# Optimization experiments

Measured on AMD Instinct MI355X. Metric: run time of the kernel, lower is better.

Reference implementation:

```python
import jax, jax.numpy as jnp
import numpy as np

B, L, H, N = 4, 4096, 1024, 16
EPS = 1e-6  # layer_norm_epsilon


def setup_inputs() -> dict:
    key = jax.random.key(0)
    ks = jax.random.split(key, 8)
    hidden_states = jax.random.normal(ks[0], (B, L, H), dtype=jnp.float32)
    attention_mask = jnp.ones((B, L), dtype=jnp.float32)
    norm_weight = jnp.ones((H,), dtype=jnp.float32)
    # S4D init: dt log-uniform in [1e-3, 1e-1]; S4D-Lin A init; random C, D
    dt_min, dt_max = 1e-3, 1e-1
    log_dt = jax.random.uniform(ks[1], (H,), dtype=jnp.float32) * (
        float(np.log(dt_max)) - float(np.log(dt_min))) + float(np.log(dt_min))
    log_A_real = jnp.log(0.5 * jnp.ones((H, N), dtype=jnp.float32))
    A_imag = jnp.broadcast_to(float(np.pi) * jnp.arange(N, dtype=jnp.float32), (H, N))
    C_real = jax.random.normal(ks[2], (H, N), dtype=jnp.float32) * (0.5 ** 0.5)
    C_imag = jax.random.normal(ks[3], (H, N), dtype=jnp.float32) * (0.5 ** 0.5)
    D = jax.random.normal(ks[4], (H,), dtype=jnp.float32)
    out_w = jax.random.normal(ks[5], (2 * H, H), dtype=jnp.float32) * 0.02  # 1x1 conv to 2H (GLU)
    out_b = jnp.zeros((2 * H,), dtype=jnp.float32)
    return dict(hidden_states=hidden_states, attention_mask=attention_mask,
                norm_weight=norm_weight, log_dt=log_dt, log_A_real=log_A_real,
                A_imag=A_imag, C_real=C_real, C_imag=C_imag, D=D,
                out_w=out_w, out_b=out_b)


def _s4d_kernel(log_dt, log_A_real, A_imag, C_real, C_imag, length):
    """Diagonal SSM convolution kernel k[h, l] (S4D ZOH discretization)."""
    dt = jnp.exp(log_dt)                                   # (H,)
    A = -jnp.exp(log_A_real) + 1j * A_imag                 # (H, N) complex64
    C = C_real + 1j * C_imag                               # (H, N)
    dtA = A * dt[:, None]                                  # (H, N)
    C_disc = C * (jnp.exp(dtA) - 1.0) / A                  # (H, N)
    vand = jnp.exp(dtA[:, :, None] * jnp.arange(length, dtype=jnp.float32))  # (H, N, L)
    k = 2.0 * jnp.einsum('hn,hnl->hl', C_disc, vand).real  # (H, L)
    return k.astype(jnp.float32)


def reference(hidden_states, attention_mask, norm_weight, log_dt, log_A_real,
              A_imag, C_real, C_imag, D, out_w, out_b):
    # LongT5LayerNorm: RMSNorm (no mean subtraction), variance in fp32
    var = jnp.mean(jnp.square(hidden_states.astype(jnp.float32)), axis=-1, keepdims=True)
    normed = hidden_states * jax.lax.rsqrt(var + EPS) * norm_weight  # (B, L, H)
    # mask padded positions, go to channel-major layout (B, H, L)
    u = (normed * attention_mask[..., None]).transpose(0, 2, 1)
    Lx = u.shape[-1]
    k = _s4d_kernel(log_dt, log_A_real, A_imag, C_real, C_imag, Lx)  # (H, L)
    # causal convolution via FFT of length 2L
    nfft = 2 * Lx
    k_f = jnp.fft.rfft(k, n=nfft)                 # (H, nfft//2+1)
    u_f = jnp.fft.rfft(u, n=nfft)                 # (B, H, nfft//2+1)
    y = jnp.fft.irfft(u_f * k_f, n=nfft)[..., :Lx]  # (B, H, L)
    y = y + u * D[:, None]                        # skip connection
    y = jax.nn.gelu(y, approximate=False)         # torch nn.GELU (exact)
    # output 1x1 conv to 2H, then GLU over the channel dim
    z = jnp.einsum('bhl,oh->bol', y, out_w) + out_b[:, None]
    a, b = jnp.split(z, 2, axis=1)
    ssm_out = (a * jax.nn.sigmoid(b)).transpose(0, 2, 1)  # (B, L, H)
    # residual + dropout (eval mode -> identity)
    return hidden_states + ssm_out
```

## Files before the change

kernel.cpp:

```cpp
#include <hip/hip_runtime.h>

#define B_   4
#define L_   4096
#define H_   1024
#define N_   16
#define CH_  64
#define NC_  (L_/CH_)
#define M_   (B_*L_)
#define O2_  (2*H_)
#define EPS_ 1e-6f

typedef __attribute__((ext_vector_type(4))) float  f32x4;
typedef __attribute__((ext_vector_type(8))) __bf16 bf16x8;

__device__ __forceinline__ unsigned short f2bf(float x) {
  union { float f; unsigned int u; } v; v.f = x;
  unsigned int r = v.u + 0x7FFFu + ((v.u >> 16) & 1u);
  return (unsigned short)(r >> 16);
}
__device__ __forceinline__ float bf2f(unsigned short x) {
  union { unsigned int u; float f; } v; v.u = ((unsigned int)x) << 16;
  return v.f;
}

__device__ __forceinline__ void async_copy16(const void* g, void* l) {
  __builtin_amdgcn_global_load_lds(
      (const __attribute__((address_space(1))) unsigned int*)g,
      (__attribute__((address_space(3))) unsigned int*)l, 16, 0, 0);
}

__global__ void k_prep(const float* __restrict__ log_dt,
                       const float* __restrict__ log_A_real,
                       const float* __restrict__ A_imag,
                       const float* __restrict__ C_real,
                       const float* __restrict__ C_imag,
                       const float* __restrict__ outw,
                       const float* __restrict__ outb,
                       float* __restrict__ wr,  float* __restrict__ wi,
                       float* __restrict__ c2r, float* __restrict__ c2i,
                       float* __restrict__ wpr, float* __restrict__ wpi,
                       unsigned short* __restrict__ Wbf,
                       float* __restrict__ bp) {
  int idx = blockIdx.x * 256 + threadIdx.x;
  int p = idx >> 10, hh = idx & (H_ - 1);
  size_t src = (size_t)((p >> 1) + (p & 1) * H_) * H_ + hh;
  Wbf[idx] = f2bf(outw[src]);
  if (idx < O2_) bp[idx] = outb[(idx >> 1) + (idx & 1) * H_];
  if (idx < H_ * N_) {
    int h = idx / N_, n = idx % N_;
    int hn = h * N_ + n;
    float dt  = expf(log_dt[h]);
    float Ar  = -expf(log_A_real[hn]);
    float Ai  = A_imag[hn];
    float dr  = Ar * dt, di = Ai * dt;
    float er  = expf(dr);
    float wrv = er * cosf(di), wiv = er * sinf(di);
    float e1r = wrv - 1.0f, e1i = wiv;
    float den = Ar * Ar + Ai * Ai;
    float qr  = (e1r * Ar + e1i * Ai) / den;
    float qi  = (e1i * Ar - e1r * Ai) / den;
    float Cr  = C_real[hn], Ci = C_imag[hn];
    float cdr = Cr * qr - Ci * qi;
    float cdi = Cr * qi + Ci * qr;
    float ep  = expf((float)CH_ * dr);
    int o = n * H_ + h;
    wr[o]  = wrv;  wi[o]  = wiv;
    c2r[o] = 2.0f * cdr; c2i[o] = 2.0f * cdi;
    wpr[o] = ep * cosf((float)CH_ * di);
    wpi[o] = ep * sinf((float)CH_ * di);
  }
}

__global__ __launch_bounds__(256) void k_scale(const float* __restrict__ hs,
                                               const float* __restrict__ mask,
                                               float* __restrict__ scale) {
  int m = blockIdx.x, tid = threadIdx.x;
  float4 v = reinterpret_cast<const float4*>(hs + (size_t)m * H_)[tid];
  float s = v.x * v.x + v.y * v.y + v.z * v.z + v.w * v.w;
  #pragma unroll
  for (int off = 32; off > 0; off >>= 1) s += __shfl_down(s, off, 64);
  __shared__ float ps[4];
  if ((tid & 63) == 0) ps[tid >> 6] = s;
  __syncthreads();
  if (tid == 0) {
    float var = (ps[0] + ps[1] + ps[2] + ps[3]) * (1.0f / H_);
    scale[m] = rsqrtf(var + EPS_) * mask[m];
  }
}

__global__ __launch_bounds__(256) void k_scan1(const float* __restrict__ hs,
                                               const float* __restrict__ nw,
                                               const float* __restrict__ scale,
                                               const float* __restrict__ wr_,
                                               const float* __restrict__ wi_,
                                               float* __restrict__ endr,
                                               float* __restrict__ endi,
                                               unsigned short* __restrict__ ubf) {
  int tid = threadIdx.x;
  int h = blockIdx.x * 256 + tid;
  int c = blockIdx.y, b = blockIdx.z;
  float wr[N_], wi[N_], xr[N_], xi[N_];
  #pragma unroll
  for (int n = 0; n < N_; n++) {
    wr[n] = wr_[n * H_ + h]; wi[n] = wi_[n * H_ + h];
    xr[n] = 0.f; xi[n] = 0.f;
  }
  float nwh = nw[h];
  int l0 = c * CH_;
  const float* scp = scale + (size_t)b * L_ + l0;
  const float* hp = hs + ((size_t)b * L_ + l0) * H_ + h;
  unsigned short* up = ubf + ((size_t)b * L_ + l0) * H_ + h;
  #pragma unroll 8
  for (int l = 0; l < CH_; l++) {
    float u = hp[(size_t)l * H_] * scp[l] * nwh;
    unsigned short ub = f2bf(u);
    up[(size_t)l * H_] = ub;
    u = bf2f(ub);
    #pragma unroll
    for (int n = 0; n < N_; n++) {
      float oxr = xr[n];
      xr[n] = fmaf(wr[n], oxr, fmaf(-wi[n], xi[n], u));
      xi[n] = fmaf(wr[n], xi[n], wi[n] * oxr);
    }
  }
  size_t base = (((size_t)b * NC_ + c) * N_) * H_ + h;
  #pragma unroll
  for (int n = 0; n < N_; n++) {
    endr[base + (size_t)n * H_] = xr[n];
    endi[base + (size_t)n * H_] = xi[n];
  }
}

__global__ __launch_bounds__(256) void k_carry(const float* __restrict__ wpr_,
                                               const float* __restrict__ wpi_,
                                               const float* __restrict__ endr,
                                               const float* __restrict__ endi,
                                               float* __restrict__ carr,
                                               float* __restrict__ cari) {
  int idx = blockIdx.x * 256 + threadIdx.x;
  int h = idx & (H_ - 1);
  int n = (idx >> 10) & (N_ - 1);
  int b = idx >> 14;
  float wprv = wpr_[n * H_ + h], wpiv = wpi_[n * H_ + h];
  float sr = 0.f, si = 0.f;
  size_t cstride = (size_t)N_ * H_;
  size_t base = ((size_t)b * NC_) * cstride + (size_t)n * H_ + h;
  for (int c = 0; c < NC_; c++, base += cstride) {
    carr[base] = sr; cari[base] = si;
    float er = endr[base], ei = endi[base];
    float osr = sr;
    sr = fmaf(wprv, osr,  fmaf(-wpiv, si, er));
    si = fmaf(wprv, si, fmaf(wpiv, osr, ei));
  }
}

__global__ __launch_bounds__(256) void k_scan2(const unsigned short* __restrict__ ubf,
                                               const float* __restrict__ wr_,
                                               const float* __restrict__ wi_,
                                               const float* __restrict__ c2r_,
                                               const float* __restrict__ c2i_,
                                               const float* __restrict__ Dp,
                                               const float* __restrict__ carr,
                                               const float* __restrict__ cari,
                                               unsigned short* __restrict__ ybf) {
  __shared__ __align__(16) unsigned short us[CH_ * 256];
  int tid = threadIdx.x;
  int hb = blockIdx.x;
  int c = blockIdx.y, b = blockIdx.z;
  int h = hb * 256 + tid;
  int l0 = c * CH_;
  const unsigned short* usrc = ubf + ((size_t)b * L_ + l0) * H_ + hb * 256;
  #pragma unroll
  for (int i = 0; i < 8; i++) {
    int g = i * 256 + tid;
    int l = g >> 5, hq = (g & 31) * 8;
    async_copy16(usrc + (size_t)l * H_ + hq, &us[g * 8]);
  }
  __syncthreads();

  float yacc[CH_];
  float Dh = Dp[h];
  #pragma unroll
  for (int l = 0; l < CH_; l++)
    yacc[l] = Dh * bf2f(us[l * 256 + tid]);

  size_t base = (((size_t)b * NC_ + c) * N_) * H_ + h;
  for (int n = 0; n < N_; n++) {
    float wrv = wr_[n * H_ + h],  wiv = wi_[n * H_ + h];
    float crv = c2r_[n * H_ + h], civ = c2i_[n * H_ + h];
    float xr = carr[base + (size_t)n * H_];
    float xi = cari[base + (size_t)n * H_];
    #pragma unroll
    for (int l = 0; l < CH_; l++) {
      float u = bf2f(us[l * 256 + tid]);
      float oxr = xr;
      xr = fmaf(wrv, oxr, fmaf(-wiv, xi, u));
      xi = fmaf(wrv, xi, wiv * oxr);
      yacc[l] = fmaf(crv, xr, fmaf(-civ, xi, yacc[l]));
    }
  }
  unsigned short* yp = ybf + ((size_t)b * L_ + l0) * H_ + h;
  #pragma unroll
  for (int l = 0; l < CH_; l++) {
    float yv = yacc[l];
    float g = 0.5f * yv * (1.0f + erff(yv * 0.70710678118654752f));
    yp[(size_t)l * H_] = f2bf(g);
  }
}

#define BM 128
#define BN 128
#define BKG 64
#define GSTRIDE 68
__global__ __launch_bounds__(256) void k_gemm(const unsigned short* __restrict__ A,
                                              const unsigned short* __restrict__ Bw,
                                              const float* __restrict__ bp,
                                              const float* __restrict__ hs,
                                              float* __restrict__ out) {
  __shared__ __align__(16) char smem[BM * GSTRIDE * 4];
  unsigned short* As = (unsigned short*)smem;
  unsigned short* Bs = As + BM * BKG;
  float* gt = (float*)smem;
  const int tid  = threadIdx.x;
  const int lane = tid & 63;
  const int wave = tid >> 6;
  const int bn = blockIdx.x * BN;
  const int bm = blockIdx.y * BM;
  const int wm = (wave >> 1) * 64;
  const int wn = (wave & 1) * 64;
  const int K = H_;
  f32x4 acc[4][4];
  #pragma unroll
  for (int mi = 0; mi < 4; mi++)
    #pragma unroll
    for (int ni = 0; ni < 4; ni++) acc[mi][ni] = (f32x4){0.f, 0.f, 0.f, 0.f};

  int rr[4], cc[4];
  #pragma unroll
  for (int i = 0; i < 4; i++) {
    int g = i * 256 + tid;
    rr[i] = g >> 3;
    cc[i] = ((g & 7) ^ (rr[i] & 7)) * 8;
  }
  const int ar = lane & 15, kqi = lane >> 4;

  for (int k0 = 0; k0 < K; k0 += BKG) {
    #pragma unroll
    for (int i = 0; i < 4; i++)
      async_copy16(A + (size_t)(bm + rr[i]) * K + k0 + cc[i], &As[(i * 256 + tid) * 8]);
    #pragma unroll
    for (int i = 0; i < 4; i++)
      async_copy16(Bw + (size_t)(bn + rr[i]) * K + k0 + cc[i], &Bs[(i * 256 + tid) * 8]);
    __syncthreads();
    #pragma unroll
    for (int kh = 0; kh < 2; kh++) {
      bf16x8 af[4], bf[4];
      #pragma unroll
      for (int mi = 0; mi < 4; mi++) {
        int row = wm + mi * 16 + ar;
        af[mi] = *reinterpret_cast<const bf16x8*>(
            &As[row * BKG + (((kh * 4 + kqi) ^ (row & 7)) * 8)]);
      }
      #pragma unroll
      for (int ni = 0; ni < 4; ni++) {
        int row = wn + ni * 16 + ar;
        bf[ni] = *reinterpret_cast<const bf16x8*>(
            &Bs[row * BKG + (((kh * 4 + kqi) ^ (row & 7)) * 8)]);
      }
      #pragma unroll
      for (int mi = 0; mi < 4; mi++)
        #pragma unroll
        for (int ni = 0; ni < 4; ni++)
          acc[mi][ni] = __builtin_amdgcn_mfma_f32_16x16x32_bf16(af[mi], bf[ni], acc[mi][ni], 0, 0, 0);
    }
    __syncthreads();
  }

  #pragma unroll
  for (int ni = 0; ni < 4; ni++) {
    int p  = wn + ni * 16 + (lane & 15);
    int pe = (bn + p) & ~1;
    float bA = bp[pe], bB = bp[pe + 1];
    int jl = p >> 1;
    #pragma unroll
    for (int mi = 0; mi < 4; mi++) {
      int row0 = wm + mi * 16 + (lane >> 4) * 4;
      #pragma unroll
      for (int r = 0; r < 4; r++) {
        float v = acc[mi][ni][r];
        float w = __shfl_xor(v, 1, 64);
        if (!(lane & 1))
          gt[(row0 + r) * GSTRIDE + jl] = (v + bA) / (1.0f + __expf(-(w + bB)));
      }
    }
  }
  __syncthreads();
  {
    const int c4 = tid & 15;
    const int rw = tid >> 4;
    const size_t obase = (size_t)bm * H_ + (bn >> 1);
    #pragma unroll
    for (int rep = 0; rep < 8; rep++) {
      int row = rep * 16 + rw;
      float4 g = *reinterpret_cast<const float4*>(&gt[row * GSTRIDE + c4 * 4]);
      size_t o = obase + (size_t)row * H_ + c4 * 4;
      float4 hv = *reinterpret_cast<const float4*>(&hs[o]);
      float4 rv = {hv.x + g.x, hv.y + g.y, hv.z + g.z, hv.w + g.w};
      *reinterpret_cast<float4*>(&out[o]) = rv;
    }
  }
}

extern "C" void kernel_launch(void* const* d_in, const int* in_sizes, int n_in,
                              void* d_out, int out_size, void* d_ws, size_t ws_size,
                              hipStream_t stream) {
  const float* hs    = (const float*)d_in[0];
  const float* mask  = (const float*)d_in[1];
  const float* nw    = (const float*)d_in[2];
  const float* ldt   = (const float*)d_in[3];
  const float* lar   = (const float*)d_in[4];
  const float* aim   = (const float*)d_in[5];
  const float* crl   = (const float*)d_in[6];
  const float* cim   = (const float*)d_in[7];
  const float* Dp    = (const float*)d_in[8];
  const float* outw  = (const float*)d_in[9];
  const float* outb  = (const float*)d_in[10];
  float* out = (float*)d_out;

  size_t off = 0;
  char* ws = (char*)d_ws;
  auto nxt = [&](size_t bytes) -> void* {
    void* p = ws + off; off += (bytes + 255) & ~(size_t)255; return p;
  };
  float* wr   = (float*)nxt(H_ * N_ * 4);
  float* wi   = (float*)nxt(H_ * N_ * 4);
  float* c2r  = (float*)nxt(H_ * N_ * 4);
  float* c2i  = (float*)nxt(H_ * N_ * 4);
  float* wpr  = (float*)nxt(H_ * N_ * 4);
  float* wpi  = (float*)nxt(H_ * N_ * 4);
  float* bpck = (float*)nxt(O2_ * 4);
  float* scale= (float*)nxt((size_t)M_ * 4);
  float* endr = (float*)nxt((size_t)B_ * NC_ * N_ * H_ * 4);
  float* endi = (float*)nxt((size_t)B_ * NC_ * N_ * H_ * 4);
  float* carr = (float*)nxt((size_t)B_ * NC_ * N_ * H_ * 4);
  float* cari = (float*)nxt((size_t)B_ * NC_ * N_ * H_ * 4);
  unsigned short* Wbf = (unsigned short*)nxt((size_t)O2_ * H_ * 2);
  unsigned short* ubf = (unsigned short*)nxt((size_t)M_ * H_ * 2);
  unsigned short* ybf = (unsigned short*)nxt((size_t)M_ * H_ * 2);

  k_prep<<<dim3(O2_ * H_ / 256), dim3(256), 0, stream>>>(ldt, lar, aim, crl, cim,
                                                         outw, outb,
                                                         wr, wi, c2r, c2i, wpr, wpi,
                                                         Wbf, bpck);
  k_scale<<<dim3(M_), dim3(256), 0, stream>>>(hs, mask, scale);
  k_scan1<<<dim3(H_ / 256, NC_, B_), dim3(256), 0, stream>>>(hs, nw, scale, wr, wi,
                                                             endr, endi, ubf);
  k_carry<<<dim3(B_ * N_ * H_ / 256), dim3(256), 0, stream>>>(wpr, wpi, endr, endi, carr, cari);
  k_scan2<<<dim3(H_ / 256, NC_, B_), dim3(256), 0, stream>>>(ubf, wr, wi, c2r, c2i,
                                                             Dp, carr, cari, ybf);
  k_gemm<<<dim3(O2_ / BN, M_ / BM), dim3(256), 0, stream>>>(ybf, Wbf, bpck, hs, out);
}
```

Baseline: 356.2 us.

## Rewrite output GEMM as 256x256 tile with double-buffered, phase-interleaved async loads

Replaces the 128x128 single-buffered bf16 MFMA GEMM with a 256x256 tile run by 512 threads. It uses 128KB of dynamic LDS holding two buffers and splits each K-step into eight phases, so global-to-LDS copies for later tiles are issued while MFMAs run on the current tile. Waits are fine-grained through vmcnt and raw barriers, with setprio around the MFMAs. The aim is to hide load latency and raise operand reuse per byte loaded. The cost is a fragile hand-tuned schedule, less parallelism from a smaller grid, and an epilogue split into two halves.

```diff
diff --git a/kernel.cpp b/kernel.cpp
--- a/kernel.cpp
+++ b/kernel.cpp
@@ -208,106 +208,167 @@
   }
 }
 
-#define BM 128
-#define BN 128
-#define BKG 64
-#define GSTRIDE 68
-__global__ __launch_bounds__(256) void k_gemm(const unsigned short* __restrict__ A,
-                                              const unsigned short* __restrict__ Bw,
-                                              const float* __restrict__ bp,
-                                              const float* __restrict__ hs,
-                                              float* __restrict__ out) {
-  __shared__ __align__(16) char smem[BM * GSTRIDE * 4];
-  unsigned short* As = (unsigned short*)smem;
-  unsigned short* Bs = As + BM * BKG;
-  float* gt = (float*)smem;
+#define BM2 256
+#define BN2 256
+#define NT2 16
+#define GST 132
+#define GEMM_LDS 131072
+
+#define STAGE_A(buf, half, kt) do { \
+  async_copy16(Ag + (size_t)(bm + rp0 + ((half) << 6)) * H_ + (kt) * 64 + ca0, \
+               sA + (buf) * 32768 + ((half) << 13) + tid * 16); \
+  async_copy16(Ag + (size_t)(bm + rp1 + 64 + ((half) << 6)) * H_ + (kt) * 64 + ca1, \
+               sA + (buf) * 32768 + ((half) << 13) + 16384 + tid * 16); \
+} while (0)
+
+#define STAGE_B(buf, eo, kt) do { \
+  async_copy16(Bg + (size_t)(bn + ((rp0 >> 5) << 6) + (rp0 & 31) + ((eo) << 5)) * H_ + (kt) * 64 + ca0, \
+               sB + (buf) * 32768 + ((rp0 >> 5) << 13) + ((rp0 & 31) << 7) + ((eo) << 12) + (q0 << 4)); \
+  async_copy16(Bg + (size_t)(bn + ((rp1 >> 5) << 6) + (rp1 & 31) + ((eo) << 5)) * H_ + (kt) * 64 + ca1, \
+               sB + (buf) * 32768 + ((rp1 >> 5) << 13) + ((rp1 & 31) << 7) + ((eo) << 12) + (q0 << 4)); \
+} while (0)
+
+#define VM4  asm volatile("s_waitcnt vmcnt(4)" ::: "memory")
+#define NOVM do {} while (0)
+
+#define PHASE(buf, mh, nh, STAGE_STMT, CLOSE_STMT) do { \
+  bf16x8 af[4][2], bfr[2][2]; \
+  _Pragma("unroll") \
+  for (int m2 = 0; m2 < 4; m2++) { \
+    _Pragma("unroll") \
+    for (int kk = 0; kk < 2; kk++) \
+      af[m2][kk] = *reinterpret_cast<const bf16x8*>( \
+          sA + (buf) * 32768 + (((wm << 7) + ((mh) << 6) + (m2 << 4)) << 7) + aoff[kk]); \
+  } \
+  _Pragma("unroll") \
+  for (int n2 = 0; n2 < 2; n2++) { \
+    _Pragma("unroll") \
+    for (int kk = 0; kk < 2; kk++) \
+      bfr[n2][kk] = *reinterpret_cast<const bf16x8*>( \
+          sB + (buf) * 32768 + (((wn << 6) + ((nh) << 5) + (n2 << 4)) << 7) + aoff[kk]); \
+  } \
+  STAGE_STMT; \
+  asm volatile("" ::: "memory"); \
+  __builtin_amdgcn_s_barrier(); \
+  asm volatile("s_waitcnt lgkmcnt(0)" ::: "memory"); \
+  __builtin_amdgcn_sched_barrier(0); \
+  __builtin_amdgcn_s_setprio(1); \
+  _Pragma("unroll") \
+  for (int m2 = 0; m2 < 4; m2++) { \
+    _Pragma("unroll") \
+    for (int n2 = 0; n2 < 2; n2++) { \
+      _Pragma("unroll") \
+      for (int kk = 0; kk < 2; kk++) \
+        acc[(mh) * 4 + m2][(nh) * 2 + n2] = __builtin_amdgcn_mfma_f32_16x16x32_bf16( \
+            af[m2][kk], bfr[n2][kk], acc[(mh) * 4 + m2][(nh) * 2 + n2], 0, 0, 0); \
+    } \
+  } \
+  __builtin_amdgcn_s_setprio(0); \
+  CLOSE_STMT; \
+  asm volatile("" ::: "memory"); \
+  __builtin_amdgcn_s_barrier(); \
+  asm volatile("" ::: "memory"); \
+} while (0)
+
+__global__ __launch_bounds__(512, 2) void k_gemm(const unsigned short* __restrict__ Ag,
+                                                 const unsigned short* __restrict__ Bg,
+                                                 const float* __restrict__ bp,
+                                                 const float* __restrict__ hs,
+                                                 float* __restrict__ out) {
+  extern __shared__ __align__(16) char smem[];
+  char* sA = smem;
+  char* sB = smem + 65536;
   const int tid  = threadIdx.x;
   const int lane = tid & 63;
   const int wave = tid >> 6;
-  const int bn = blockIdx.x * BN;
-  const int bm = blockIdx.y * BM;
-  const int wm = (wave >> 1) * 64;
-  const int wn = (wave & 1) * 64;
-  const int K = H_;
-  f32x4 acc[4][4];
-  #pragma unroll
-  for (int mi = 0; mi < 4; mi++)
+  const int wm = wave >> 2;
+  const int wn = wave & 3;
+  const int bn = blockIdx.x * BN2;
+  const int bm = blockIdx.y * BM2;
+  const int ar = lane & 15, kqi = lane >> 4;
+
+  const int rp0 = tid >> 3, q0 = tid & 7;
+  const int rp1 = rp0 + 64;
+  const int ca0 = (q0 ^ (rp0 & 7)) * 8;
+  const int ca1 = (q0 ^ (rp1 & 7)) * 8;
+  int aoff[2];
+  #pragma unroll
+  for (int kk = 0; kk < 2; kk++)
+    aoff[kk] = ar * 128 + (((kk * 4 + kqi) ^ (ar & 7)) << 4);
+
+  f32x4 acc[8][4];
+  #pragma unroll
+  for (int mi = 0; mi < 8; mi++)
     #pragma unroll
     for (int ni = 0; ni < 4; ni++) acc[mi][ni] = (f32x4){0.f, 0.f, 0.f, 0.f};
 
-  int rr[4], cc[4];
-  #pragma unroll
-  for (int i = 0; i < 4; i++) {
-    int g = i * 256 + tid;
-    rr[i] = g >> 3;
-    cc[i] = ((g & 7) ^ (rr[i] & 7)) * 8;
-  }
-  const int ar = lane & 15, kqi = lane >> 4;
-
-  for (int k0 = 0; k0 < K; k0 += BKG) {
-    #pragma unroll
-    for (int i = 0; i < 4; i++)
-      async_copy16(A + (size_t)(bm + rr[i]) * K + k0 + cc[i], &As[(i * 256 + tid) * 8]);
-    #pragma unroll
-    for (int i = 0; i < 4; i++)
-      async_copy16(Bw + (size_t)(bn + rr[i]) * K + k0 + cc[i], &Bs[(i * 256 + tid) * 8]);
-    __syncthreads();
-    #pragma unroll
-    for (int kh = 0; kh < 2; kh++) {
-      bf16x8 af[4], bf[4];
-      #pragma unroll
-      for (int mi = 0; mi < 4; mi++) {
-        int row = wm + mi * 16 + ar;
-        af[mi] = *reinterpret_cast<const bf16x8*>(
-            &As[row * BKG + (((kh * 4 + kqi) ^ (row & 7)) * 8)]);
-      }
+  STAGE_A(0, 0, 0);
+  STAGE_B(0, 0, 0);
+  STAGE_A(0, 1, 0);
+  STAGE_B(0, 1, 0);
+  STAGE_A(1, 0, 1);
+  STAGE_B(1, 1, 1);
+  VM4;
+  __builtin_amdgcn_s_barrier();
+  asm volatile("" ::: "memory");
+
+  #pragma unroll 1
+  for (int i = 0; i < NT2 / 2; i++) {
+    const int tb = 2 * i + 1;
+    const int tc = (2 * i + 2 < NT2) ? 2 * i + 2 : NT2 - 1;
+    const int td = (2 * i + 3 < NT2) ? 2 * i + 3 : NT2 - 1;
+    PHASE(0, 0, 0, STAGE_A(1, 1, tb), NOVM);
+    PHASE(0, 0, 1, STAGE_B(1, 0, tb), NOVM);
+    PHASE(0, 1, 1, STAGE_A(0, 0, tc), NOVM);
+    PHASE(0, 1, 0, STAGE_B(0, 1, tc), VM4);
+    PHASE(1, 0, 0, STAGE_A(0, 1, tc), NOVM);
+    PHASE(1, 0, 1, STAGE_B(0, 0, tc), NOVM);
+    PHASE(1, 1, 1, STAGE_A(1, 0, td), NOVM);
+    PHASE(1, 1, 0, STAGE_B(1, 1, td), VM4);
+  }
+  asm volatile("s_waitcnt vmcnt(0)" ::: "memory");
+  __builtin_amdgcn_s_barrier();
+  asm volatile("" ::: "memory");
+
+  float* gt = (float*)smem;
+  #pragma unroll
+  for (int hf = 0; hf < 2; hf++) {
+    if (wm == hf) {
       #pragma unroll
       for (int ni = 0; ni < 4; ni++) {
-        int row = wn + ni * 16 + ar;
-        bf[ni] = *reinterpret_cast<const bf16x8*>(
-            &Bs[row * BKG + (((kh * 4 + kqi) ^ (row & 7)) * 8)]);
+        int p  = wn * 64 + ni * 16 + (lane & 15);
+        int pe = (bn + p) & ~1;
+        float bA = bp[pe], bB = bp[pe + 1];
+        int jl = p >> 1;
+        #pragma unroll
+        for (int mi = 0; mi < 8; mi++) {
+          int lrow0 = mi * 16 + (lane >> 4) * 4;
+          #pragma unroll
+          for (int r = 0; r < 4; r++) {
+            float v = acc[mi][ni][r];
+            float w = __shfl_xor(v, 1, 64);
+            if (!(lane & 1))
+              gt[(lrow0 + r) * GST + jl] = (v + bA) / (1.0f + __expf(-(w + bB)));
+          }
+        }
       }
-      #pragma unroll
-      for (int mi = 0; mi < 4; mi++)
-        #pragma unroll
-        for (int ni = 0; ni < 4; ni++)
-          acc[mi][ni] = __builtin_amdgcn_mfma_f32_16x16x32_bf16(af[mi], bf[ni], acc[mi][ni], 0, 0, 0);
     }
     __syncthreads();
-  }
-
-  #pragma unroll
-  for (int ni = 0; ni < 4; ni++) {
-    int p  = wn + ni * 16 + (lane & 15);
-    int pe = (bn + p) & ~1;
-    float bA = bp[pe], bB = bp[pe + 1];
-    int jl = p >> 1;
-    #pragma unroll
-    for (int mi = 0; mi < 4; mi++) {
-      int row0 = wm + mi * 16 + (lane >> 4) * 4;
+    {
+      const int c4 = tid & 31;
+      const int rw = tid >> 5;
+      const size_t obase = (size_t)(bm + hf * 128) * H_ + (bn >> 1);
       #pragma unroll
-      for (int r = 0; r < 4; r++) {
-        float v = acc[mi][ni][r];
-        float w = __shfl_xor(v, 1, 64);
-        if (!(lane & 1))
-          gt[(row0 + r) * GSTRIDE + jl] = (v + bA) / (1.0f + __expf(-(w + bB)));
+      for (int rep = 0; rep < 8; rep++) {
+        int row = rep * 16 + rw;
+        float4 g = *reinterpret_cast<const float4*>(&gt[row * GST + c4 * 4]);
+        size_t o = obase + (size_t)row * H_ + c4 * 4;
+        float4 hv = *reinterpret_cast<const float4*>(&hs[o]);
+        float4 rv = {hv.x + g.x, hv.y + g.y, hv.z + g.z, hv.w + g.w};
+        *reinterpret_cast<float4*>(&out[o]) = rv;
       }
     }
-  }
-  __syncthreads();
-  {
-    const int c4 = tid & 15;
-    const int rw = tid >> 4;
-    const size_t obase = (size_t)bm * H_ + (bn >> 1);
-    #pragma unroll
-    for (int rep = 0; rep < 8; rep++) {
-      int row = rep * 16 + rw;
-      float4 g = *reinterpret_cast<const float4*>(&gt[row * GSTRIDE + c4 * 4]);
-      size_t o = obase + (size_t)row * H_ + c4 * 4;
-      float4 hv = *reinterpret_cast<const float4*>(&hs[o]);
-      float4 rv = {hv.x + g.x, hv.y + g.y, hv.z + g.z, hv.w + g.w};
-      *reinterpret_cast<float4*>(&out[o]) = rv;
-    }
+    __syncthreads();
   }
 }
 
@@ -326,6 +387,13 @@
   const float* outw  = (const float*)d_in[9];
   const float* outb  = (const float*)d_in[10];
   float* out = (float*)d_out;
+
+  static bool attr_done = false;
+  if (!attr_done) {
+    hipFuncSetAttribute((const void*)k_gemm,
+                        hipFuncAttributeMaxDynamicSharedMemorySize, GEMM_LDS);
+    attr_done = true;
+  }
 
   size_t off = 0;
   char* ws = (char*)d_ws;
@@ -358,5 +426,5 @@
   k_carry<<<dim3(B_ * N_ * H_ / 256), dim3(256), 0, stream>>>(wpr, wpi, endr, endi, carr, cari);
   k_scan2<<<dim3(H_ / 256, NC_, B_), dim3(256), 0, stream>>>(ubf, wr, wi, c2r, c2i,
                                                              Dp, carr, cari, ybf);
-  k_gemm<<<dim3(O2_ / BN, M_ / BM), dim3(256), 0, stream>>>(ybf, Wbf, bpck, hs, out);
-}
+  k_gemm<<<dim3(O2_ / BN2, M_ / BM2), dim3(512), GEMM_LDS, stream>>>(ybf, Wbf, bpck, hs, out);
+}
```

New measurement: 371.9 us. 1.04x slower.
